# Optimization experiments

Measured on AMD Instinct MI355X. Metric: run time of the kernel, lower is better.

The kernel has to match this reference:

```python
import jax, jax.numpy as jnp
import numpy as np

N_NODES = 50000
N_EDGES = 800000
NUM_HEADS = 4
HEAD_DIM = 32
IN_DIM = 128
NEG_SLOPE = 0.2


def setup_inputs() -> dict:
    key = jax.random.key(0)
    k1, k2, k3, k4, k5, k6 = jax.random.split(key, 6)
    x = jax.random.normal(k1, (N_NODES, IN_DIM), dtype=jnp.float32)
    W = jax.random.normal(k2, (NUM_HEADS * HEAD_DIM, IN_DIM), dtype=jnp.float32) * 0.05
    attn_l = jax.random.normal(k3, (NUM_HEADS, HEAD_DIM), dtype=jnp.float32) * 0.05
    attn_r = jax.random.normal(k4, (NUM_HEADS, HEAD_DIM), dtype=jnp.float32) * 0.05
    src = jax.random.randint(k5, (N_EDGES,), 0, N_NODES, dtype=jnp.int32)
    dst = jnp.sort(jax.random.randint(k6, (N_EDGES,), 0, N_NODES, dtype=jnp.int32))
    return {"x": x, "W": W, "attn_l": attn_l, "attn_r": attn_r, "src": src, "dst": dst}


def reference(x, W, attn_l, attn_r, src, dst):
    N = x.shape[0]
    H, D = attn_l.shape
    # linear projection: [N, H*D] -> [N, H, D]
    feat = (x @ W.T).reshape(N, H, D)
    # per-node attention terms  [N, H]
    el = jnp.einsum('nhd,hd->nh', feat, attn_l)
    er = jnp.einsum('nhd,hd->nh', feat, attn_r)
    # per-edge logits (u_add_v) + leaky relu  [E, H]
    e = el[src] + er[dst]
    e = jnp.where(e > 0, e, NEG_SLOPE * e)
    # edge softmax segmented by destination node
    e_max = jax.ops.segment_max(e, dst, num_segments=N)          # [N, H]
    e_exp = jnp.exp(e - e_max[dst])                              # [E, H]
    denom = jax.ops.segment_sum(e_exp, dst, num_segments=N)     # [N, H]
    alpha = e_exp / denom[dst]                                   # [E, H]
    # attention-weighted neighbor aggregation  [N, H, D]
    out = jax.ops.segment_sum(alpha[:, :, None] * feat[src], dst, num_segments=N)
    return out.reshape(N, H * D)
```

## Files before the change

### kernel.cpp

```cpp
#include <hip/hip_runtime.h>
#include <math.h>

#define NN 50000
#define NE 800000
#define NH 4
#define HD 32
#define FD 128
#define NTILE 3125

typedef __attribute__((ext_vector_type(8))) short short8;
typedef __attribute__((ext_vector_type(4))) float floatx4;

__device__ __forceinline__ unsigned short f2bf(float f) {
    union { float f; unsigned u; } v; v.f = f;
    unsigned u = v.u;
    return (unsigned short)((u + 0x7FFFu + ((u >> 16) & 1u)) >> 16);
}
__device__ __forceinline__ float bf_lo(unsigned u) {
    union { unsigned u; float f; } v; v.u = u << 16; return v.f;
}
__device__ __forceinline__ float bf_hi(unsigned u) {
    union { unsigned u; float f; } v; v.u = u & 0xFFFF0000u; return v.f;
}

__global__ __launch_bounds__(512) void k_gemm_fused(const float* __restrict__ x,
                                                    const float* __restrict__ W,
                                                    const float* __restrict__ al,
                                                    const float* __restrict__ ar,
                                                    const int* __restrict__ dst,
                                                    unsigned short* __restrict__ feat_bf,
                                                    float* __restrict__ el,
                                                    float* __restrict__ er,
                                                    int* __restrict__ rows) {
    __shared__ unsigned short Wl[FD * 136];
    __shared__ unsigned short ABl[16 * 136];
    const int tid = threadIdx.x;

    for (int p = tid; p < FD * 64; p += 512) {
        int c = p >> 6, k2 = (p & 63) * 2;
        float2 wv = *(const float2*)&W[c * FD + k2];
        *(unsigned*)&Wl[c * 136 + k2] =
            (unsigned)f2bf(wv.x) | ((unsigned)f2bf(wv.y) << 16);
    }
    for (int p = tid; p < 16 * 128; p += 512) {
        int j = p >> 7, k = p & 127;
        float g = 0.f;
        if (j < 8) {
            int hh = j & 3;
            const float* av = (j < 4) ? al : ar;
            #pragma unroll
            for (int d = 0; d < 32; ++d)
                g += av[hh * 32 + d] * W[(size_t)(hh * 32 + d) * FD + k];
        }
        ABl[j * 136 + k] = f2bf(g);
    }
    __syncthreads();

    const int wv_id = tid >> 6, lane = tid & 63;
    const int col = lane & 15, quad = lane >> 4;

    for (int tile = blockIdx.x * 8 + wv_id; tile < NTILE; tile += gridDim.x * 8) {
        const int n0 = tile * 16;

        short8 afrag[4];
        const float* xrow = x + (size_t)(n0 + col) * FD;
        #pragma unroll
        for (int s = 0; s < 4; ++s) {
            float4 u0 = *(const float4*)&xrow[s * 32 + quad * 8];
            float4 u1 = *(const float4*)&xrow[s * 32 + quad * 8 + 4];
            short8 a;
            a[0] = (short)f2bf(u0.x); a[1] = (short)f2bf(u0.y);
            a[2] = (short)f2bf(u0.z); a[3] = (short)f2bf(u0.w);
            a[4] = (short)f2bf(u1.x); a[5] = (short)f2bf(u1.y);
            a[6] = (short)f2bf(u1.z); a[7] = (short)f2bf(u1.w);
            afrag[s] = a;
        }

        floatx4 acc[8];
        floatx4 accE = (floatx4){0.f, 0.f, 0.f, 0.f};
        #pragma unroll
        for (int ct = 0; ct < 8; ++ct) acc[ct] = (floatx4){0.f, 0.f, 0.f, 0.f};

        #pragma unroll
        for (int ct = 0; ct < 8; ++ct) {
            #pragma unroll
            for (int s = 0; s < 4; ++s) {
                short8 b = *(const short8*)&Wl[(ct * 16 + col) * 136 + s * 32 + quad * 8];
                acc[ct] = __builtin_amdgcn_mfma_f32_16x16x32_bf16(afrag[s], b, acc[ct], 0, 0, 0);
            }
        }
        #pragma unroll
        for (int s = 0; s < 4; ++s) {
            short8 b = *(const short8*)&ABl[col * 136 + s * 32 + quad * 8];
            accE = __builtin_amdgcn_mfma_f32_16x16x32_bf16(afrag[s], b, accE, 0, 0, 0);
        }

        #pragma unroll
        for (int ct = 0; ct < 8; ++ct) {
            #pragma unroll
            for (int r = 0; r < 4; ++r) {
                feat_bf[(size_t)(n0 + quad * 4 + r) * FD + ct * 16 + col] = f2bf(acc[ct][r]);
            }
        }
        if (col < 8) {
            float* base = (col < 4) ? el : er;
            int hh = col & 3;
            #pragma unroll
            for (int r = 0; r < 4; ++r)
                base[(n0 + quad * 4 + r) * NH + hh] = accE[r];
        }
    }

    const int gsz = gridDim.x * 512;
    for (int i = blockIdx.x * 512 + tid; i < NE; i += gsz) {
        int cur = dst[i];
        if (i == 0) {
            for (int n = 0; n <= cur; ++n) rows[n] = 0;
        } else {
            int prev = dst[i - 1];
            for (int n = prev + 1; n <= cur; ++n) rows[n] = i;
        }
        if (i == NE - 1) {
            for (int n = cur + 1; n <= NN; ++n) rows[n] = NE;
        }
    }
}

__global__ __launch_bounds__(256) void k_aggregate(const unsigned short* __restrict__ feat_bf,
                                                   const float* __restrict__ el,
                                                   const float* __restrict__ er,
                                                   const int* __restrict__ src,
                                                   const int* __restrict__ rows,
                                                   float* __restrict__ out) {
    const int wave = threadIdx.x >> 6;
    const int lane = threadIdx.x & 63;
    const int n = blockIdx.x * 4 + wave;
    if (n >= NN) return;

    const int s = rows[n], t = rows[n + 1];
    const int q  = lane >> 4;
    const int lp = lane & 15;
    const int h  = lp >> 2;
    const int dimoff = 8 * lp;

    const float erh = er[n * NH + h];

    float acc[8] = {0.f, 0.f, 0.f, 0.f, 0.f, 0.f, 0.f, 0.f};
    float den = 0.f;

    for (int e = s; e < t; e += 16) {
        int sjv[4];
        #pragma unroll
        for (int u = 0; u < 4; ++u) {
            int ei = e + 4 * u + q;
            sjv[u] = src[(ei < t) ? ei : (t - 1)];
        }
        float elv[4];
        #pragma unroll
        for (int u = 0; u < 4; ++u) elv[u] = el[sjv[u] * NH + h];
        uint4 uvv[4];
        #pragma unroll
        for (int u = 0; u < 4; ++u)
            uvv[u] = *(const uint4*)&feat_bf[(size_t)sjv[u] * FD + dimoff];
        #pragma unroll
        for (int u = 0; u < 4; ++u) {
            int ei = e + 4 * u + q;
            float lg = elv[u] + erh;
            float z  = fmaxf(lg, 0.2f * lg);
            float w  = (ei < t) ? __expf(z) : 0.f;
            uint4 uv = uvv[u];
            acc[0] += w * bf_lo(uv.x); acc[1] += w * bf_hi(uv.x);
            acc[2] += w * bf_lo(uv.y); acc[3] += w * bf_hi(uv.y);
            acc[4] += w * bf_lo(uv.z); acc[5] += w * bf_hi(uv.z);
            acc[6] += w * bf_lo(uv.w); acc[7] += w * bf_hi(uv.w);
            den += w;
        }
    }

    #pragma unroll
    for (int m = 16; m < 64; m <<= 1) {
        #pragma unroll
        for (int j = 0; j < 8; ++j) acc[j] += __shfl_xor(acc[j], m);
        den += __shfl_xor(den, m);
    }

    if (q == 0) {
        const float rden = (den > 0.f) ? 1.f / den : 0.f;
        float* op = out + (size_t)n * FD + dimoff;
        *(float4*)op       = make_float4(acc[0] * rden, acc[1] * rden, acc[2] * rden, acc[3] * rden);
        *(float4*)(op + 4) = make_float4(acc[4] * rden, acc[5] * rden, acc[6] * rden, acc[7] * rden);
    }
}

extern "C" void kernel_launch(void* const* d_in, const int* in_sizes, int n_in,
                              void* d_out, int out_size, void* d_ws, size_t ws_size,
                              hipStream_t stream) {
    const float* x  = (const float*)d_in[0];
    const float* W  = (const float*)d_in[1];
    const float* al = (const float*)d_in[2];
    const float* ar = (const float*)d_in[3];
    const int* src  = (const int*)d_in[4];
    const int* dst  = (const int*)d_in[5];
    float* out = (float*)d_out;

    unsigned short* feat_bf = (unsigned short*)d_ws;
    float* el = (float*)(feat_bf + (size_t)NN * FD);
    float* er = el + (size_t)NN * NH;
    int*   rows = (int*)(er + (size_t)NN * NH);

    k_gemm_fused<<<256, 512, 0, stream>>>(x, W, al, ar, dst, feat_bf, el, er, rows);
    k_aggregate<<<(NN + 3) / 4, 256, 0, stream>>>(feat_bf, el, er, src, rows, out);
}
```

Baseline: 138.6 us.

## Split pipeline into prep, gemm, edge-weight and two-node aggregation kernels

Moves the attention-vector folding into a small prep kernel so each GEMM block no longer recomputes it, and doubles the GEMM grid. Edge logits and exp weights are now computed once per edge in a separate kernel that also builds the CSR row offsets, storing per-edge weights in workspace. The aggregation kernel handles two destination nodes per wave, interleaving their gathers to raise memory-level parallelism. In exchange it adds two kernel launches and a round trip of 12.8MB of edge weights through memory.

```diff
diff --git a/kernel.cpp b/kernel.cpp
--- a/kernel.cpp
+++ b/kernel.cpp
@@ -23,15 +23,30 @@
     union { unsigned u; float f; } v; v.u = u & 0xFFFF0000u; return v.f;
 }
 
-__global__ __launch_bounds__(512) void k_gemm_fused(const float* __restrict__ x,
-                                                    const float* __restrict__ W,
-                                                    const float* __restrict__ al,
-                                                    const float* __restrict__ ar,
-                                                    const int* __restrict__ dst,
-                                                    unsigned short* __restrict__ feat_bf,
-                                                    float* __restrict__ el,
-                                                    float* __restrict__ er,
-                                                    int* __restrict__ rows) {
+__global__ void k_prep(const float* __restrict__ W,
+                       const float* __restrict__ al,
+                       const float* __restrict__ ar,
+                       unsigned short* __restrict__ Gbf) {
+    int p = blockIdx.x * blockDim.x + threadIdx.x;
+    if (p >= 16 * 128) return;
+    int j = p >> 7, k = p & 127;
+    float g = 0.f;
+    if (j < 8) {
+        int hh = j & 3;
+        const float* av = (j < 4) ? al : ar;
+        #pragma unroll
+        for (int d = 0; d < 32; ++d)
+            g += av[hh * 32 + d] * W[(size_t)(hh * 32 + d) * FD + k];
+    }
+    Gbf[p] = f2bf(g);
+}
+
+__global__ __launch_bounds__(512) void k_gemm(const float* __restrict__ x,
+                                              const float* __restrict__ W,
+                                              const unsigned short* __restrict__ Gbf,
+                                              unsigned short* __restrict__ feat_bf,
+                                              float* __restrict__ el,
+                                              float* __restrict__ er) {
     __shared__ unsigned short Wl[FD * 136];
     __shared__ unsigned short ABl[16 * 136];
     const int tid = threadIdx.x;
@@ -44,15 +59,7 @@
     }
     for (int p = tid; p < 16 * 128; p += 512) {
         int j = p >> 7, k = p & 127;
-        float g = 0.f;
-        if (j < 8) {
-            int hh = j & 3;
-            const float* av = (j < 4) ? al : ar;
-            #pragma unroll
-            for (int d = 0; d < 32; ++d)
-                g += av[hh * 32 + d] * W[(size_t)(hh * 32 + d) * FD + k];
-        }
-        ABl[j * 136 + k] = f2bf(g);
+        ABl[j * 136 + k] = Gbf[p];
     }
     __syncthreads();
 
@@ -110,85 +117,144 @@
                 base[(n0 + quad * 4 + r) * NH + hh] = accE[r];
         }
     }
-
-    const int gsz = gridDim.x * 512;
-    for (int i = blockIdx.x * 512 + tid; i < NE; i += gsz) {
-        int cur = dst[i];
-        if (i == 0) {
-            for (int n = 0; n <= cur; ++n) rows[n] = 0;
-        } else {
-            int prev = dst[i - 1];
-            for (int n = prev + 1; n <= cur; ++n) rows[n] = i;
-        }
-        if (i == NE - 1) {
-            for (int n = cur + 1; n <= NN; ++n) rows[n] = NE;
-        }
-    }
+}
+
+__global__ void k_edgew(const float* __restrict__ el,
+                        const float* __restrict__ er,
+                        const int* __restrict__ src,
+                        const int* __restrict__ dst,
+                        float* __restrict__ wP,
+                        int* __restrict__ rows) {
+    int e = blockIdx.x * blockDim.x + threadIdx.x;
+    if (e >= NE) return;
+    int sj = src[e], dj = dst[e];
+
+    if (e == 0) {
+        for (int n = 0; n <= dj; ++n) rows[n] = 0;
+    } else {
+        int prev = dst[e - 1];
+        for (int n = prev + 1; n <= dj; ++n) rows[n] = e;
+    }
+    if (e == NE - 1) {
+        for (int n = dj + 1; n <= NN; ++n) rows[n] = NE;
+    }
+
+    float4 el4 = *(const float4*)&el[sj * NH];
+    float4 er4 = *(const float4*)&er[dj * NH];
+    float4 w;
+    float lg, z;
+    lg = el4.x + er4.x; z = fmaxf(lg, 0.2f * lg); w.x = __expf(z);
+    lg = el4.y + er4.y; z = fmaxf(lg, 0.2f * lg); w.y = __expf(z);
+    lg = el4.z + er4.z; z = fmaxf(lg, 0.2f * lg); w.z = __expf(z);
+    lg = el4.w + er4.w; z = fmaxf(lg, 0.2f * lg); w.w = __expf(z);
+    *(float4*)&wP[e * NH] = w;
 }
 
 __global__ __launch_bounds__(256) void k_aggregate(const unsigned short* __restrict__ feat_bf,
-                                                   const float* __restrict__ el,
-                                                   const float* __restrict__ er,
+                                                   const float* __restrict__ wP,
                                                    const int* __restrict__ src,
                                                    const int* __restrict__ rows,
                                                    float* __restrict__ out) {
     const int wave = threadIdx.x >> 6;
     const int lane = threadIdx.x & 63;
-    const int n = blockIdx.x * 4 + wave;
-    if (n >= NN) return;
-
-    const int s = rows[n], t = rows[n + 1];
+    const int pair = blockIdx.x * 4 + wave;
+    const int n0 = pair * 2;
+    if (n0 >= NN) return;
+    const int n1 = n0 + 1;
+
     const int q  = lane >> 4;
     const int lp = lane & 15;
     const int h  = lp >> 2;
     const int dimoff = 8 * lp;
 
-    const float erh = er[n * NH + h];
-
-    float acc[8] = {0.f, 0.f, 0.f, 0.f, 0.f, 0.f, 0.f, 0.f};
-    float den = 0.f;
-
-    for (int e = s; e < t; e += 16) {
-        int sjv[4];
-        #pragma unroll
-        for (int u = 0; u < 4; ++u) {
-            int ei = e + 4 * u + q;
-            sjv[u] = src[(ei < t) ? ei : (t - 1)];
-        }
-        float elv[4];
-        #pragma unroll
-        for (int u = 0; u < 4; ++u) elv[u] = el[sjv[u] * NH + h];
-        uint4 uvv[4];
-        #pragma unroll
-        for (int u = 0; u < 4; ++u)
-            uvv[u] = *(const uint4*)&feat_bf[(size_t)sjv[u] * FD + dimoff];
-        #pragma unroll
-        for (int u = 0; u < 4; ++u) {
-            int ei = e + 4 * u + q;
-            float lg = elv[u] + erh;
-            float z  = fmaxf(lg, 0.2f * lg);
-            float w  = (ei < t) ? __expf(z) : 0.f;
-            uint4 uv = uvv[u];
-            acc[0] += w * bf_lo(uv.x); acc[1] += w * bf_hi(uv.x);
-            acc[2] += w * bf_lo(uv.y); acc[3] += w * bf_hi(uv.y);
-            acc[4] += w * bf_lo(uv.z); acc[5] += w * bf_hi(uv.z);
-            acc[6] += w * bf_lo(uv.w); acc[7] += w * bf_hi(uv.w);
-            den += w;
+    const int s0 = rows[n0], t0 = rows[n0 + 1];
+    const int s1 = rows[n1], t1 = rows[n1 + 1];
+
+    float acc0[8] = {0.f,0.f,0.f,0.f,0.f,0.f,0.f,0.f};
+    float acc1[8] = {0.f,0.f,0.f,0.f,0.f,0.f,0.f,0.f};
+    float den0 = 0.f, den1 = 0.f;
+
+    int e0 = s0, e1 = s1;
+    while ((e0 < t0) || (e1 < t1)) {
+        const bool a0 = e0 < t0, a1 = e1 < t1;
+        int   sj0[4], sj1[4];
+        float w0[4],  w1[4];
+        if (a0) {
+            #pragma unroll
+            for (int u = 0; u < 4; ++u) {
+                int ei = e0 + 4 * u + q;
+                int ec = (ei < t0) ? ei : (t0 - 1);
+                sj0[u] = src[ec];
+                w0[u]  = (ei < t0) ? wP[ec * NH + h] : 0.f;
+            }
+        }
+        if (a1) {
+            #pragma unroll
+            for (int u = 0; u < 4; ++u) {
+                int ei = e1 + 4 * u + q;
+                int ec = (ei < t1) ? ei : (t1 - 1);
+                sj1[u] = src[ec];
+                w1[u]  = (ei < t1) ? wP[ec * NH + h] : 0.f;
+            }
+        }
+        uint4 f0[4], f1[4];
+        if (a0) {
+            #pragma unroll
+            for (int u = 0; u < 4; ++u)
+                f0[u] = *(const uint4*)&feat_bf[(size_t)sj0[u] * FD + dimoff];
+        }
+        if (a1) {
+            #pragma unroll
+            for (int u = 0; u < 4; ++u)
+                f1[u] = *(const uint4*)&feat_bf[(size_t)sj1[u] * FD + dimoff];
+        }
+        if (a0) {
+            #pragma unroll
+            for (int u = 0; u < 4; ++u) {
+                float w = w0[u]; uint4 uv = f0[u];
+                acc0[0] += w * bf_lo(uv.x); acc0[1] += w * bf_hi(uv.x);
+                acc0[2] += w * bf_lo(uv.y); acc0[3] += w * bf_hi(uv.y);
+                acc0[4] += w * bf_lo(uv.z); acc0[5] += w * bf_hi(uv.z);
+                acc0[6] += w * bf_lo(uv.w); acc0[7] += w * bf_hi(uv.w);
+                den0 += w;
+            }
+            e0 += 16;
+        }
+        if (a1) {
+            #pragma unroll
+            for (int u = 0; u < 4; ++u) {
+                float w = w1[u]; uint4 uv = f1[u];
+                acc1[0] += w * bf_lo(uv.x); acc1[1] += w * bf_hi(uv.x);
+                acc1[2] += w * bf_lo(uv.y); acc1[3] += w * bf_hi(uv.y);
+                acc1[4] += w * bf_lo(uv.z); acc1[5] += w * bf_hi(uv.z);
+                acc1[6] += w * bf_lo(uv.w); acc1[7] += w * bf_hi(uv.w);
+                den1 += w;
+            }
+            e1 += 16;
         }
     }
 
     #pragma unroll
     for (int m = 16; m < 64; m <<= 1) {
         #pragma unroll
-        for (int j = 0; j < 8; ++j) acc[j] += __shfl_xor(acc[j], m);
-        den += __shfl_xor(den, m);
+        for (int j = 0; j < 8; ++j) {
+            acc0[j] += __shfl_xor(acc0[j], m);
+            acc1[j] += __shfl_xor(acc1[j], m);
+        }
+        den0 += __shfl_xor(den0, m);
+        den1 += __shfl_xor(den1, m);
     }
 
     if (q == 0) {
-        const float rden = (den > 0.f) ? 1.f / den : 0.f;
-        float* op = out + (size_t)n * FD + dimoff;
-        *(float4*)op       = make_float4(acc[0] * rden, acc[1] * rden, acc[2] * rden, acc[3] * rden);
-        *(float4*)(op + 4) = make_float4(acc[4] * rden, acc[5] * rden, acc[6] * rden, acc[7] * rden);
+        const float rd = (den0 > 0.f) ? 1.f / den0 : 0.f;
+        float* op = out + (size_t)n0 * FD + dimoff;
+        *(float4*)op       = make_float4(acc0[0] * rd, acc0[1] * rd, acc0[2] * rd, acc0[3] * rd);
+        *(float4*)(op + 4) = make_float4(acc0[4] * rd, acc0[5] * rd, acc0[6] * rd, acc0[7] * rd);
+    } else if (q == 1) {
+        const float rd = (den1 > 0.f) ? 1.f / den1 : 0.f;
+        float* op = out + (size_t)n1 * FD + dimoff;
+        *(float4*)op       = make_float4(acc1[0] * rd, acc1[1] * rd, acc1[2] * rd, acc1[3] * rd);
+        *(float4*)(op + 4) = make_float4(acc1[4] * rd, acc1[5] * rd, acc1[6] * rd, acc1[7] * rd);
     }
 }
 
@@ -207,7 +273,11 @@
     float* el = (float*)(feat_bf + (size_t)NN * FD);
     float* er = el + (size_t)NN * NH;
     int*   rows = (int*)(er + (size_t)NN * NH);
-
-    k_gemm_fused<<<256, 512, 0, stream>>>(x, W, al, ar, dst, feat_bf, el, er, rows);
-    k_aggregate<<<(NN + 3) / 4, 256, 0, stream>>>(feat_bf, el, er, src, rows, out);
-}
+    float* wP = (float*)(((uintptr_t)(rows + NN + 1) + 15) & ~(uintptr_t)15);
+    unsigned short* Gbf = (unsigned short*)(wP + (size_t)NE * NH);
+
+    k_prep<<<8, 256, 0, stream>>>(W, al, ar, Gbf);
+    k_gemm<<<512, 512, 0, stream>>>(x, W, Gbf, feat_bf, el, er);
+    k_edgew<<<(NE + 255) / 256, 256, 0, stream>>>(el, er, src, dst, wP, rows);
+    k_aggregate<<<(NN / 2 + 3) / 4, 256, 0, stream>>>(feat_bf, wP, src, rows, out);
+}
```

After: 149.4 us. 7.8% more time.
